# Optimization experiments

Measured on AMD Instinct MI355X. Metric: run time of the kernel, lower is better.

## Reference

```python
import jax, jax.numpy as jnp
import numpy as np

BS, NQ, L = 64, 900, 1024
LANG_DIM, HID = 768, 256
N_EXP, TOP_K = 8, 2
MOE_W = 0.5
LOG_SCALE0 = 0.0
PRIOR_PROB = 0.01
BIAS0 = -np.log((1.0 - PRIOR_PROB) / PRIOR_PROB)  # -log((1-p)/p)


def setup_inputs() -> dict:
    key = jax.random.key(0)
    ks = jax.random.split(key, 8)
    s_in = 1.0 / np.sqrt(LANG_DIM)
    return {
        "x": jax.random.normal(ks[0], (BS, NQ, HID), jnp.float32),
        "embedding": jax.random.normal(ks[1], (BS, L, LANG_DIM), jnp.float32),
        "proj_w": jax.random.uniform(ks[2], (LANG_DIM, HID), jnp.float32, -s_in, s_in),
        "proj_b": jnp.zeros((HID,), jnp.float32),
        "gate_w": jax.random.uniform(ks[3], (LANG_DIM, N_EXP), jnp.float32, -s_in, s_in),
        "gate_b": jnp.zeros((N_EXP,), jnp.float32),
        "expert_w": jax.random.uniform(ks[4], (N_EXP, LANG_DIM, HID), jnp.float32, -s_in, s_in),
        "expert_b": jnp.zeros((N_EXP, HID), jnp.float32),
        "bias_lang": jnp.zeros((LANG_DIM,), jnp.float32),
        "bias0": jnp.array([BIAS0], jnp.float32),
        "log_scale": jnp.array([LOG_SCALE0], jnp.float32),
    }


def _moe(emb, gate_w, gate_b, expert_w, expert_b):
    # emb: (bs, L, lang_dim)
    gate_logits = emb @ gate_w + gate_b              # (bs, L, E)
    gate_weights = jax.nn.softmax(gate_logits, axis=-1)
    topv, topi = jax.lax.top_k(gate_weights, TOP_K)  # (bs, L, k)
    # dense combine weights: scatter top-k probs back to (bs, L, E)
    combine = jnp.sum(jax.nn.one_hot(topi, N_EXP, dtype=emb.dtype) * topv[..., None], axis=-2)
    out = jnp.zeros(emb.shape[:-1] + (HID,), emb.dtype)
    for e in range(N_EXP):  # small fixed expert count; dense per-expert GEMM
        out = out + combine[..., e:e + 1] * (emb @ expert_w[e] + expert_b[e])
    return out


def reference(x, embedding, proj_w, proj_b, gate_w, gate_b,
              expert_w, expert_b, bias_lang, bias0, log_scale):
    emb = embedding / jnp.linalg.norm(embedding, axis=-1, keepdims=True)
    tokens = emb @ proj_w + proj_b                        # (bs, L, HID)
    moe_out = _moe(emb, gate_w, gate_b, expert_w, expert_b)
    tokens = (1.0 - MOE_W) * tokens + MOE_W * moe_out
    token_bias = emb @ bias_lang + bias0[0]               # (bs, L)
    logit = jnp.einsum('bqh,blh->bql', x, tokens) / jnp.exp(log_scale[0])
    logit = logit + token_bias[:, None, :]
    logit = jnp.clip(logit, -50000.0, 50000.0)
    return logit
```

## Files before the change

kernel.cpp:

```cpp
#include <hip/hip_runtime.h>
#include <hip/hip_bf16.h>


typedef __attribute__((ext_vector_type(8))) short bf16x8;
typedef __attribute__((ext_vector_type(4))) float f32x4;

#define NROW 65536
#define CAP  65536
#define CSTRIDE 16
#define SWZ(r) ((((r) & 3) ^ (((r) >> 2) & 3)))

#define NB_K1 2048
#define NB_KX 14400
#define NB_K0 432
#define NB_KZ 9

__device__ __forceinline__ unsigned short f2bf(float f) {
    unsigned u = __builtin_bit_cast(unsigned, f);
    u += 0x7fffu + ((u >> 16) & 1u);
    return (unsigned short)(u >> 16);
}
__device__ __forceinline__ float bf2f(unsigned short h) {
    unsigned u = ((unsigned)h) << 16;
    return __builtin_bit_cast(float, u);
}
__device__ __forceinline__ void gload16(const void* g, void* l) {
    __builtin_amdgcn_global_load_lds(
        (const __attribute__((address_space(1))) void*)g,
        (__attribute__((address_space(3))) void*)l, 16, 0, 0);
}
__device__ __forceinline__ unsigned cvt_pk_bf16(float a, float b) {
    unsigned r;
    asm("v_cvt_pk_bf16_f32 %0, %1, %2" : "=v"(r) : "v"(a), "v"(b));
    return r;
}

__global__ __launch_bounds__(256, 4) void k_front(
    const float* __restrict__ x, const float* __restrict__ emb_in,
    const float* __restrict__ proj_w, const float* __restrict__ proj_b,
    const float* __restrict__ gate_w, const float* __restrict__ gate_b,
    const float* __restrict__ expert_w, const float* __restrict__ expert_b,
    const float* __restrict__ bias_lang, const float* __restrict__ bias0,
    unsigned short* __restrict__ x_bf, unsigned short* __restrict__ wcatT,
    float* __restrict__ bcat, unsigned* __restrict__ cnt,
    unsigned short* __restrict__ emb_bf, unsigned* __restrict__ top2,
    float2* __restrict__ c2, float* __restrict__ tbias)
{
    __shared__ __align__(16) float smem[9 * 768];
    int bid = blockIdx.x, tid = threadIdx.x;

    if (bid < NB_K1) {
        float* gwT = smem;
        for (int i = tid; i < 768 * 8; i += 256) {
            int d = i >> 3, e = i & 7;
            gwT[e * 768 + d] = gate_w[i];
        }
        for (int i = tid; i < 768; i += 256)
            gwT[8 * 768 + i] = bias_lang[i];
        __syncthreads();

        int w = tid >> 6, lane = tid & 63;
        #pragma unroll 1
        for (int it = 0; it < 8; ++it) {
            int r = bid * 32 + w * 8 + it;
            const float4* rv = (const float4*)(emb_in + (size_t)r * 768);
            float4 v0 = rv[lane], v1 = rv[lane + 64], v2 = rv[lane + 128];
            float ss = v0.x*v0.x + v0.y*v0.y + v0.z*v0.z + v0.w*v0.w
                     + v1.x*v1.x + v1.y*v1.y + v1.z*v1.z + v1.w*v1.w
                     + v2.x*v2.x + v2.y*v2.y + v2.z*v2.z + v2.w*v2.w;
            #pragma unroll
            for (int m = 1; m < 64; m <<= 1) ss += __shfl_xor(ss, m, 64);
            float rn = rsqrtf(ss);

            unsigned long long q0 = (unsigned long long)cvt_pk_bf16(v0.x*rn, v0.y*rn) |
                                    ((unsigned long long)cvt_pk_bf16(v0.z*rn, v0.w*rn) << 32);
            unsigned long long q1 = (unsigned long long)cvt_pk_bf16(v1.x*rn, v1.y*rn) |
                                    ((unsigned long long)cvt_pk_bf16(v1.z*rn, v1.w*rn) << 32);
            unsigned long long q2 = (unsigned long long)cvt_pk_bf16(v2.x*rn, v2.y*rn) |
                                    ((unsigned long long)cvt_pk_bf16(v2.z*rn, v2.w*rn) << 32);
            unsigned long long* ob = (unsigned long long*)(emb_bf + (size_t)r * 768);
            __builtin_nontemporal_store(q0, ob + lane);
            __builtin_nontemporal_store(q1, ob + lane + 64);
            __builtin_nontemporal_store(q2, ob + lane + 128);

            float acc[9];
            #pragma unroll
            for (int i = 0; i < 9; i++) acc[i] = 0.f;
            const float4 vv[3] = { v0, v1, v2 };
            #pragma unroll
            for (int k = 0; k < 3; k++) {
                float4 v = vv[k];
                #pragma unroll
                for (int e = 0; e < 9; e++) {
                    float4 g = *(const float4*)&gwT[e * 768 + k * 256 + lane * 4];
                    acc[e] += v.x*g.x + v.y*g.y + v.z*g.z + v.w*g.w;
                }
            }
            #pragma unroll
            for (int m = 1; m < 64; m <<= 1) {
                #pragma unroll
                for (int i = 0; i < 9; i++) acc[i] += __shfl_xor(acc[i], m, 64);
            }
            if (lane == 0) {
                float g[8];
                #pragma unroll
                for (int e = 0; e < 8; e++) g[e] = acc[e] * rn + gate_b[e];
                float mx = g[0];
                #pragma unroll
                for (int e = 1; e < 8; e++) mx = fmaxf(mx, g[e]);
                float p[8], s = 0.f;
                #pragma unroll
                for (int e = 0; e < 8; e++) { p[e] = __expf(g[e] - mx); s += p[e]; }
                float inv = 0.5f / s;
                int i1 = 0;
                #pragma unroll
                for (int e = 1; e < 8; e++) if (g[e] > g[i1]) i1 = e;
                int i2 = (i1 == 0) ? 1 : 0;
                #pragma unroll
                for (int e = 0; e < 8; e++) if (e != i1 && g[e] > g[i2]) i2 = e;
                top2[r] = (unsigned)i1 | ((unsigned)i2 << 8);
                c2[r]   = make_float2(p[i1] * inv, p[i2] * inv);
                tbias[r] = acc[8] * rn + bias0[0];
            }
        }
    } else if (bid < NB_K1 + NB_KX) {
        int i = (bid - NB_K1) * 256 + tid;
        float4 v = ((const float4*)x)[i];
        unsigned long long o = (unsigned long long)cvt_pk_bf16(v.x, v.y) |
                               ((unsigned long long)cvt_pk_bf16(v.z, v.w) << 32);
        __builtin_nontemporal_store(o, (unsigned long long*)x_bf + i);
    } else if (bid < NB_K1 + NB_KX + NB_K0) {
        int u = bid - NB_K1 - NB_KX;
        int j = u / 48, rem = u % 48;
        int d0 = (rem % 12) * 64, h0 = (rem / 12) * 64;
        const float* W = (j < 8) ? expert_w + (size_t)j * 768 * 256 : proj_w;
        unsigned short (*s)[65] = (unsigned short (*)[65])smem;
        #pragma unroll
        for (int i = 0; i < 16; i++) {
            int d = i * 4 + (tid >> 6), h = tid & 63;
            s[d][h] = f2bf(W[(size_t)(d0 + d) * 256 + h0 + h]);
        }
        __syncthreads();
        #pragma unroll
        for (int i = 0; i < 16; i++) {
            int h = i * 4 + (tid >> 6), d = tid & 63;
            wcatT[(size_t)(j * 256 + h0 + h) * 768 + d0 + d] = s[d][h];
        }
    } else {
        int i = (bid - NB_K1 - NB_KX - NB_K0) * 256 + tid;
        if (i < 2304) {
            int jj = i >> 8, h = i & 255;
            bcat[i] = (jj < 8) ? expert_b[jj * 256 + h] : proj_b[h];
        }
        if (i < 8 * CSTRIDE) cnt[i] = 0;
    }
}

__global__ __launch_bounds__(256) void kb_bucket(
    const unsigned* __restrict__ top2, const float2* __restrict__ c2,
    unsigned* __restrict__ cnt, unsigned* __restrict__ bidx,
    float* __restrict__ bscale)
{
    __shared__ unsigned lcnt[8];
    __shared__ unsigned gbase[8];
    int tid = threadIdx.x, lane = tid & 63;
    if (tid < 8) lcnt[tid] = 0;
    __syncthreads();
    int r = blockIdx.x * 256 + tid;
    unsigned t = top2[r];
    float2 c = c2[r];
    int ii[2] = { (int)(t & 255), (int)((t >> 8) & 255) };
    float cc[2] = { c.x, c.y };
    unsigned lpos[2];
    #pragma unroll
    for (int slot = 0; slot < 2; slot++) {
        int myE = ii[slot];
        #pragma unroll 1
        for (int e = 0; e < 8; e++) {
            unsigned long long mask = __ballot(myE == e);
            if (myE == e) {
                int leader = __ffsll((unsigned long long)mask) - 1;
                unsigned base = 0;
                if (lane == leader)
                    base = atomicAdd(&lcnt[e], (unsigned)__popcll(mask));
                base = __shfl(base, leader, 64);
                lpos[slot] = base + (unsigned)__popcll(mask & ((1ull << lane) - 1ull));
            }
        }
    }
    __syncthreads();
    if (tid < 8) gbase[tid] = atomicAdd(&cnt[tid * CSTRIDE], lcnt[tid]);
    __syncthreads();
    #pragma unroll
    for (int slot = 0; slot < 2; slot++) {
        int e = ii[slot];
        unsigned p = gbase[e] + lpos[slot];
        bidx[(size_t)e * CAP + p]   = (unsigned)r | ((unsigned)slot << 16);
        bscale[(size_t)e * CAP + p] = cc[slot];
    }
}

__global__ __launch_bounds__(512, 2) void k2_expert(
    const unsigned short* __restrict__ emb_bf, const unsigned short* __restrict__ wcatT,
    const float* __restrict__ bcat, const unsigned* __restrict__ cnt,
    const unsigned* __restrict__ bidx, const float* __restrict__ bscale,
    unsigned short* __restrict__ partial)
{
    int e = blockIdx.y;
    int tile = blockIdx.x;
    int cnt_e = (int)cnt[e * CSTRIDE];
    if (tile * 128 >= cnt_e) return;
    int tid = threadIdx.x, lane = tid & 63, w = tid >> 6;
    int wm = w >> 2, wn = w & 3;
    __shared__ __align__(16) unsigned short As[2][128 * 32];
    __shared__ __align__(16) unsigned short Bs[2][256 * 32];
    __shared__ unsigned sRow[128];
    __shared__ float sScale[128];
    if (tid < 128) {
        int gi = tile * 128 + tid;
        unsigned rs; float sc;
        if (gi < cnt_e) { rs = bidx[(size_t)e * CAP + gi];
                          sc = bscale[(size_t)e * CAP + gi]; }
        else            { rs = 0; sc = 0.f; }
        sRow[tid] = rs; sScale[tid] = sc;
    }
    __syncthreads();
    int r16 = lane & 15, r4 = lane >> 4;
    int srowA = tid >> 2, ssegA = (tid & 3) ^ SWZ(srowA);
    const unsigned short* aSrc =
        emb_bf + (size_t)(sRow[srowA] & 0xFFFFu) * 768 + ssegA * 8;
    const unsigned short* bBase = wcatT + (size_t)e * 256 * 768;

    auto stageA = [&](int kt, int buf) {
        gload16(aSrc + kt * 32, &As[buf][w * 512]);
    };
    auto stageB = [&](int kt, int buf) {
        #pragma unroll
        for (int i = 0; i < 2; i++) {
            int u = i * 512 + tid;
            int brow = u >> 2, seg = (u & 3) ^ SWZ(brow);
            gload16(&bBase[(size_t)brow * 768 + kt * 32 + seg * 8],
                    &Bs[buf][i * 4096 + w * 512]);
        }
    };

    f32x4 acc[4][4];
    #pragma unroll
    for (int mi = 0; mi < 4; mi++)
        #pragma unroll
        for (int ni = 0; ni < 4; ni++) acc[mi][ni] = f32x4{0.f, 0.f, 0.f, 0.f};

    stageA(0, 0); stageB(0, 0);
    __syncthreads();
    int buf = 0;
    #pragma unroll 1
    for (int kt = 0; kt < 24; ++kt) {
        if (kt < 23) { stageA(kt + 1, buf ^ 1); stageB(kt + 1, buf ^ 1); }
        bf16x8 a[4], b[4];
        #pragma unroll
        for (int mi = 0; mi < 4; mi++) {
            int arow = wm * 64 + mi * 16 + r16;
            a[mi] = *(const bf16x8*)&As[buf][arow * 32 + (r4 ^ SWZ(arow)) * 8];
        }
        #pragma unroll
        for (int ni = 0; ni < 4; ni++) {
            int brow = wn * 64 + ni * 16 + r16;
            b[ni] = *(const bf16x8*)&Bs[buf][brow * 32 + (r4 ^ SWZ(brow)) * 8];
        }
        #pragma unroll
        for (int mi = 0; mi < 4; mi++)
            #pragma unroll
            for (int ni = 0; ni < 4; ni++)
                acc[mi][ni] = __builtin_amdgcn_mfma_f32_16x16x32_bf16(
                    a[mi], b[ni], acc[mi][ni], 0, 0, 0);
        __syncthreads();
        buf ^= 1;
    }

    float bj[4];
    #pragma unroll
    for (int ni = 0; ni < 4; ni++) bj[ni] = bcat[e * 256 + wn * 64 + ni * 16 + r16];
    #pragma unroll
    for (int mi = 0; mi < 4; mi++) {
        #pragma unroll
        for (int e4 = 0; e4 < 4; e4++) {
            int rl = wm * 64 + mi * 16 + r4 * 4 + e4;
            if (tile * 128 + rl < cnt_e) {
                unsigned rs = sRow[rl];
                float sc = sScale[rl];
                unsigned rowg = rs & 0xFFFFu, slot = rs >> 16;
                #pragma unroll
                for (int ni = 0; ni < 4; ni++) {
                    int col = wn * 64 + ni * 16 + r16;
                    __builtin_nontemporal_store(
                        f2bf(sc * (acc[mi][ni][e4] + bj[ni])),
                        &partial[((size_t)slot * NROW + rowg) * 256 + col]);
                }
            }
        }
    }
}

__global__ __launch_bounds__(512, 2) void k2_proj(
    const unsigned short* __restrict__ emb_bf, const unsigned short* __restrict__ wcatT,
    const float* __restrict__ bcat, const unsigned short* __restrict__ partial,
    unsigned short* __restrict__ tokens)
{
    int tile = blockIdx.x;
    int tid = threadIdx.x, lane = tid & 63, w = tid >> 6;
    int wm = w >> 2, wn = w & 3;
    int rowBase = tile * 128;
    __shared__ __align__(16) unsigned short As[2][128 * 32];
    __shared__ __align__(16) unsigned short Bs[2][256 * 32];
    int r16 = lane & 15, r4 = lane >> 4;
    int srowA = tid >> 2, ssegA = (tid & 3) ^ SWZ(srowA);
    const unsigned short* aSrc =
        emb_bf + (size_t)(rowBase + srowA) * 768 + ssegA * 8;
    const unsigned short* bBase = wcatT + (size_t)8 * 256 * 768;

    auto stageA = [&](int kt, int buf) {
        gload16(aSrc + kt * 32, &As[buf][w * 512]);
    };
    auto stageB = [&](int kt, int buf) {
        #pragma unroll
        for (int i = 0; i < 2; i++) {
            int u = i * 512 + tid;
            int brow = u >> 2, seg = (u & 3) ^ SWZ(brow);
            gload16(&bBase[(size_t)brow * 768 + kt * 32 + seg * 8],
                    &Bs[buf][i * 4096 + w * 512]);
        }
    };

    f32x4 acc[4][4];
    #pragma unroll
    for (int mi = 0; mi < 4; mi++)
        #pragma unroll
        for (int ni = 0; ni < 4; ni++) acc[mi][ni] = f32x4{0.f, 0.f, 0.f, 0.f};

    stageA(0, 0); stageB(0, 0);
    __syncthreads();
    int buf = 0;
    #pragma unroll 1
    for (int kt = 0; kt < 24; ++kt) {
        if (kt < 23) { stageA(kt + 1, buf ^ 1); stageB(kt + 1, buf ^ 1); }
        bf16x8 a[4], b[4];
        #pragma unroll
        for (int mi = 0; mi < 4; mi++) {
            int arow = wm * 64 + mi * 16 + r16;
            a[mi] = *(const bf16x8*)&As[buf][arow * 32 + (r4 ^ SWZ(arow)) * 8];
        }
        #pragma unroll
        for (int ni = 0; ni < 4; ni++) {
            int brow = wn * 64 + ni * 16 + r16;
            b[ni] = *(const bf16x8*)&Bs[buf][brow * 32 + (r4 ^ SWZ(brow)) * 8];
        }
        #pragma unroll
        for (int mi = 0; mi < 4; mi++)
            #pragma unroll
            for (int ni = 0; ni < 4; ni++)
                acc[mi][ni] = __builtin_amdgcn_mfma_f32_16x16x32_bf16(
                    a[mi], b[ni], acc[mi][ni], 0, 0, 0);
        __syncthreads();
        buf ^= 1;
    }

    const size_t S = (size_t)NROW * 256;
    float bj[4];
    #pragma unroll
    for (int ni = 0; ni < 4; ni++) bj[ni] = bcat[8 * 256 + wn * 64 + ni * 16 + r16];
    #pragma unroll
    for (int mi = 0; mi < 4; mi++) {
        #pragma unroll
        for (int e4 = 0; e4 < 4; e4++) {
            int rl = wm * 64 + mi * 16 + r4 * 4 + e4;
            size_t rowg = rowBase + rl;
            #pragma unroll
            for (int ni = 0; ni < 4; ni++) {
                int col = wn * 64 + ni * 16 + r16;
                float p0 = bf2f(partial[rowg * 256 + col]);
                float p1 = bf2f(partial[S + rowg * 256 + col]);
                float v = 0.5f * (acc[mi][ni][e4] + bj[ni]) + p0 + p1;
                __builtin_nontemporal_store(f2bf(v), &tokens[rowg * 256 + col]);
            }
        }
    }
}

__global__ __launch_bounds__(256, 4) void k3_logit(
    const unsigned short* __restrict__ x_bf, const unsigned short* __restrict__ tokens,
    const float* __restrict__ tbias, const float* __restrict__ log_scale,
    float* __restrict__ out)
{
    int wgid = blockIdx.x;
    int xcd = wgid & 7, slot = wgid >> 3;
    int b = xcd + 8 * (slot >> 6);
    int t64 = slot & 63;
    int tm = t64 >> 3, tn = t64 & 7;

    int tid = threadIdx.x, lane = tid & 63, w = tid >> 6;
    int wm = w >> 1, wn = w & 1;
    __shared__ __align__(16) unsigned short As[2][128 * 32];
    __shared__ __align__(16) unsigned short Bs[2][128 * 32];
    const unsigned short* A = x_bf + (size_t)b * 900 * 256;
    const unsigned short* B = tokens + (size_t)b * 1024 * 256;
    f32x4 acc[4][4];
    #pragma unroll
    for (int mi = 0; mi < 4; mi++)
        #pragma unroll
        for (int ni = 0; ni < 4; ni++) acc[mi][ni] = f32x4{0.f, 0.f, 0.f, 0.f};
    int r16 = lane & 15, r4 = lane >> 4;

    auto stage = [&](int kt, int buf) {
        #pragma unroll
        for (int i = 0; i < 2; i++) {
            int u = i * 256 + tid;
            int row = u >> 2, seg = (u & 3) ^ SWZ(row);
            int ar = tm * 128 + row;
            if (ar > 899) ar = 899;
            gload16(&A[(size_t)ar * 256 + kt * 32 + seg * 8],
                    &As[buf][i * 2048 + w * 512]);
            int nr = tn * 128 + row;
            gload16(&B[(size_t)nr * 256 + kt * 32 + seg * 8],
                    &Bs[buf][i * 2048 + w * 512]);
        }
    };

    stage(0, 0);
    __syncthreads();
    int buf = 0;
    #pragma unroll 1
    for (int kt = 0; kt < 8; ++kt) {
        if (kt < 7) stage(kt + 1, buf ^ 1);
        bf16x8 a[4], bb[4];
        #pragma unroll
        for (int mi = 0; mi < 4; mi++) {
            int row = wm * 64 + mi * 16 + r16;
            a[mi] = *(const bf16x8*)&As[buf][row * 32 + (r4 ^ SWZ(row)) * 8];
        }
        #pragma unroll
        for (int ni = 0; ni < 4; ni++) {
            int row = wn * 64 + ni * 16 + r16;
            bb[ni] = *(const bf16x8*)&Bs[buf][row * 32 + (r4 ^ SWZ(row)) * 8];
        }
        #pragma unroll
        for (int mi = 0; mi < 4; mi++)
            #pragma unroll
            for (int ni = 0; ni < 4; ni++)
                acc[mi][ni] = __builtin_amdgcn_mfma_f32_16x16x32_bf16(
                    a[mi], bb[ni], acc[mi][ni], 0, 0, 0);
        __syncthreads();
        buf ^= 1;
    }
    float inv = __expf(-log_scale[0]);
    #pragma unroll
    for (int ni = 0; ni < 4; ni++) {
        int l = tn * 128 + wn * 64 + ni * 16 + r16;
        float tbv = tbias[b * 1024 + l];
        #pragma unroll
        for (int mi = 0; mi < 4; mi++) {
            #pragma unroll
            for (int e = 0; e < 4; e++) {
                int q = tm * 128 + wm * 64 + mi * 16 + r4 * 4 + e;
                if (q < 900) {
                    float vv = acc[mi][ni][e] * inv + tbv;
                    vv = fminf(fmaxf(vv, -50000.f), 50000.f);
                    __builtin_nontemporal_store(
                        vv, &out[((size_t)b * 900 + q) * 1024 + l]);
                }
            }
        }
    }
}

extern "C" void kernel_launch(void* const* d_in, const int* in_sizes, int n_in,
                              void* d_out, int out_size, void* d_ws, size_t ws_size,
                              hipStream_t stream)
{
    const float* x         = (const float*)d_in[0];
    const float* embedding = (const float*)d_in[1];
    const float* proj_w    = (const float*)d_in[2];
    const float* proj_b    = (const float*)d_in[3];
    const float* gate_w    = (const float*)d_in[4];
    const float* gate_b    = (const float*)d_in[5];
    const float* expert_w  = (const float*)d_in[6];
    const float* expert_b  = (const float*)d_in[7];
    const float* bias_lang = (const float*)d_in[8];
    const float* bias0     = (const float*)d_in[9];
    const float* log_scale = (const float*)d_in[10];
    float* out = (float*)d_out;

    size_t off = 0;
    char* base = (char*)d_ws;
    auto alloc = [&](size_t bytes) -> void* {
        void* p = base + off;
        off += (bytes + 255) & ~(size_t)255;
        return p;
    };
    unsigned short* emb_bf  = (unsigned short*)alloc((size_t)NROW * 768 * 2);
    unsigned short* x_bf    = (unsigned short*)alloc((size_t)14745600 * 2);
    unsigned short* wcatT   = (unsigned short*)alloc((size_t)2304 * 768 * 2);
    float* bcat             = (float*)alloc(2304 * 4);
    float* tbias            = (float*)alloc((size_t)NROW * 4);
    unsigned short* tokens  = (unsigned short*)alloc((size_t)NROW * 256 * 2);
    unsigned* cnt           = (unsigned*)alloc(8 * CSTRIDE * 4);
    unsigned* top2          = (unsigned*)alloc((size_t)NROW * 4);
    float2* c2              = (float2*)alloc((size_t)NROW * 8);
    unsigned* bidx          = (unsigned*)alloc((size_t)8 * CAP * 4);
    float* bscale           = (float*)alloc((size_t)8 * CAP * 4);
    unsigned short* partial = (unsigned short*)alloc((size_t)2 * NROW * 256 * 2);

    k_front<<<NB_K1 + NB_KX + NB_K0 + NB_KZ, 256, 0, stream>>>(
        x, embedding, proj_w, proj_b, gate_w, gate_b, expert_w, expert_b,
        bias_lang, bias0, x_bf, wcatT, bcat, cnt, emb_bf, top2, c2, tbias);
    kb_bucket<<<NROW / 256, 256, 0, stream>>>(top2, c2, cnt, bidx, bscale);
    dim3 g2(512, 8);
    k2_expert<<<g2, 512, 0, stream>>>(emb_bf, wcatT, bcat, cnt, bidx, bscale, partial);
    k2_proj<<<512, 512, 0, stream>>>(emb_bf, wcatT, bcat, partial, tokens);
    k3_logit<<<4096, 256, 0, stream>>>(x_bf, tokens, tbias, log_scale, out);
}
```

Baseline: 379.0 us.

## Stage full K extent into LDS in two halves with fewer barriers in logit GEMM

The logit GEMM kernel no longer runs an 8-step double-buffered K loop with a barrier per step. It now issues global-to-LDS loads for the whole K=256 extent up front as two 128-wide halves, using an XOR swizzle over 16 segments. It waits only for the first half before computing, then waits for the second. This removes per-step synchronisation and keeps more loads in flight. The cost is 128 KB of LDS per block and dropping the 4-blocks-per-CU launch bound, which lowers occupancy.

```diff
diff --git a/kernel.cpp b/kernel.cpp
--- a/kernel.cpp
+++ b/kernel.cpp
@@ -386,7 +386,7 @@
     }
 }
 
-__global__ __launch_bounds__(256, 4) void k3_logit(
+__global__ __launch_bounds__(256) void k3_logit(
     const unsigned short* __restrict__ x_bf, const unsigned short* __restrict__ tokens,
     const float* __restrict__ tbias, const float* __restrict__ log_scale,
     float* __restrict__ out)
@@ -399,8 +399,8 @@
 
     int tid = threadIdx.x, lane = tid & 63, w = tid >> 6;
     int wm = w >> 1, wn = w & 1;
-    __shared__ __align__(16) unsigned short As[2][128 * 32];
-    __shared__ __align__(16) unsigned short Bs[2][128 * 32];
+    __shared__ __align__(16) unsigned short As[2][128 * 128];
+    __shared__ __align__(16) unsigned short Bs[2][128 * 128];
     const unsigned short* A = x_bf + (size_t)b * 900 * 256;
     const unsigned short* B = tokens + (size_t)b * 1024 * 256;
     f32x4 acc[4][4];
@@ -410,47 +410,63 @@
         for (int ni = 0; ni < 4; ni++) acc[mi][ni] = f32x4{0.f, 0.f, 0.f, 0.f};
     int r16 = lane & 15, r4 = lane >> 4;
 
-    auto stage = [&](int kt, int buf) {
-        #pragma unroll
-        for (int i = 0; i < 2; i++) {
+    auto stageHalf = [&](int half) {
+        #pragma unroll
+        for (int i = 0; i < 8; i++) {
             int u = i * 256 + tid;
-            int row = u >> 2, seg = (u & 3) ^ SWZ(row);
+            int row = u >> 4, seg = u & 15;
+            int ps = seg ^ (row & 15);
             int ar = tm * 128 + row;
             if (ar > 899) ar = 899;
-            gload16(&A[(size_t)ar * 256 + kt * 32 + seg * 8],
-                    &As[buf][i * 2048 + w * 512]);
+            gload16(&A[(size_t)ar * 256 + half * 128 + ps * 8],
+                    &As[half][(i * 256 + w * 64) * 8]);
+        }
+        #pragma unroll
+        for (int i = 0; i < 8; i++) {
+            int u = i * 256 + tid;
+            int row = u >> 4, seg = u & 15;
+            int ps = seg ^ (row & 15);
             int nr = tn * 128 + row;
-            gload16(&B[(size_t)nr * 256 + kt * 32 + seg * 8],
-                    &Bs[buf][i * 2048 + w * 512]);
+            gload16(&B[(size_t)nr * 256 + half * 128 + ps * 8],
+                    &Bs[half][(i * 256 + w * 64) * 8]);
         }
     };
 
-    stage(0, 0);
-    __syncthreads();
-    int buf = 0;
+    stageHalf(0);
+    stageHalf(1);
+    asm volatile("s_waitcnt vmcnt(16)" ::: "memory");
+    __builtin_amdgcn_s_barrier();
+
     #pragma unroll 1
-    for (int kt = 0; kt < 8; ++kt) {
-        if (kt < 7) stage(kt + 1, buf ^ 1);
-        bf16x8 a[4], bb[4];
-        #pragma unroll
-        for (int mi = 0; mi < 4; mi++) {
-            int row = wm * 64 + mi * 16 + r16;
-            a[mi] = *(const bf16x8*)&As[buf][row * 32 + (r4 ^ SWZ(row)) * 8];
-        }
-        #pragma unroll
-        for (int ni = 0; ni < 4; ni++) {
-            int row = wn * 64 + ni * 16 + r16;
-            bb[ni] = *(const bf16x8*)&Bs[buf][row * 32 + (r4 ^ SWZ(row)) * 8];
-        }
-        #pragma unroll
-        for (int mi = 0; mi < 4; mi++)
-            #pragma unroll
-            for (int ni = 0; ni < 4; ni++)
-                acc[mi][ni] = __builtin_amdgcn_mfma_f32_16x16x32_bf16(
-                    a[mi], bb[ni], acc[mi][ni], 0, 0, 0);
-        __syncthreads();
-        buf ^= 1;
-    }
+    for (int half = 0; half < 2; ++half) {
+        #pragma unroll
+        for (int kt = 0; kt < 4; ++kt) {
+            bf16x8 a[4], bb[4];
+            #pragma unroll
+            for (int mi = 0; mi < 4; mi++) {
+                int row = wm * 64 + mi * 16 + r16;
+                a[mi] = *(const bf16x8*)&As[half][row * 128 +
+                        (((kt * 4 + r4) ^ (row & 15)) * 8)];
+            }
+            #pragma unroll
+            for (int ni = 0; ni < 4; ni++) {
+                int row = wn * 64 + ni * 16 + r16;
+                bb[ni] = *(const bf16x8*)&Bs[half][row * 128 +
+                         (((kt * 4 + r4) ^ (row & 15)) * 8)];
+            }
+            #pragma unroll
+            for (int mi = 0; mi < 4; mi++)
+                #pragma unroll
+                for (int ni = 0; ni < 4; ni++)
+                    acc[mi][ni] = __builtin_amdgcn_mfma_f32_16x16x32_bf16(
+                        a[mi], bb[ni], acc[mi][ni], 0, 0, 0);
+        }
+        if (half == 0) {
+            asm volatile("s_waitcnt vmcnt(0)" ::: "memory");
+            __builtin_amdgcn_s_barrier();
+        }
+    }
+
     float inv = __expf(-log_scale[0]);
     #pragma unroll
     for (int ni = 0; ni < 4; ni++) {
```

After: 443.3 us. 1.17x slower.
